# Optimization experiments

Measured on AMD Instinct MI355X. Metric: run time of the kernel, lower is better.

Reference implementation:

```python
import jax, jax.numpy as jnp
import numpy as np

DECAY = 0.95

def setup_inputs() -> dict:
    key = jax.random.key(0)
    k1, k2, k3, k4 = jax.random.split(key, 4)
    B, S, H, Dk, Dv = 4, 4096, 16, 64, 64
    return {
        "memory": jax.random.normal(k1, (H, Dk, Dv), dtype=jnp.float32),
        "keys": jax.random.normal(k2, (B, S, H, Dk), dtype=jnp.float32),
        "values": jax.random.normal(k3, (B, S, H, Dv), dtype=jnp.float32),
        "write_strengths": jax.random.uniform(k4, (B, S), dtype=jnp.float32),
    }

def reference(memory, keys, values, write_strengths):
    # M_new = decay * M + sum_{b,s} rho[b,s] * k[b,s,h] v[b,s,h]^T
    # Algebraically equivalent to per-head (rho-weighted) K^T V contraction;
    # avoids materializing the (B,S,H,Dk,Dv) outer-product tensor.
    delta = jnp.einsum('bs,bshk,bshv->hkv', write_strengths, keys, values)
    return DECAY * memory + delta
```

## Files before the change

### kernel.cpp

```cpp
#include <hip/hip_runtime.h>


typedef __bf16  bf16x8  __attribute__((ext_vector_type(8)));
typedef float   floatx4 __attribute__((ext_vector_type(4)));

constexpr int HH = 16;
constexpr int DK = 64;
constexpr int DV = 64;
constexpr int ROWS = 16384;
constexpr int NSLICE = 64;
constexpr int RPB = ROWS / NSLICE;
constexpr int RPW = RPB / 4;
constexpr int TS  = 32;
constexpr int NT  = RPW / TS;
constexpr int PAD = 65;
constexpr float DECAY = 0.95f;
constexpr size_t WS_NEED = (size_t)NSLICE * HH * DK * DV * 4;

__global__ __launch_bounds__(256) void init_out(const float* __restrict__ mem,
                                                float* __restrict__ out) {
    int i = blockIdx.x * 256 + threadIdx.x;
    out[i] = DECAY * mem[i];
}

__global__ __launch_bounds__(256) void accum(const float* __restrict__ keys,
                                             const float* __restrict__ values,
                                             const float* __restrict__ rho,
                                             float* __restrict__ out,
                                             float* __restrict__ ws,
                                             int use_ws) {
    __shared__ float red[2][64 * PAD];

    const int t    = threadIdx.x;
    const int w    = t >> 6;
    const int lane = t & 63;
    const int m15  = lane & 15;
    const int q    = lane >> 4;
    const int h    = blockIdx.y;
    const int row0 = blockIdx.x * RPB + w * RPW;

    floatx4 acc[4][4];
    #pragma unroll
    for (int i = 0; i < 4; ++i)
        #pragma unroll
        for (int j = 0; j < 4; ++j)
            acc[i][j] = (floatx4){0.f, 0.f, 0.f, 0.f};

    #pragma unroll
    for (int tile = 0; tile < NT; ++tile) {
        const int s0 = row0 + tile * TS;
        const int sl = s0 + q * 8;

        float4 r0 = *(const float4*)(rho + sl);
        float4 r1 = *(const float4*)(rho + sl + 4);
        float rv[8] = {r0.x, r0.y, r0.z, r0.w, r1.x, r1.y, r1.z, r1.w};

        const float* kbase = keys   + ((size_t)sl * HH + h) * DK + m15;
        const float* vbase = values + ((size_t)sl * HH + h) * DV + m15;

        bf16x8 af[4], bfr[4];
        #pragma unroll
        for (int mt = 0; mt < 4; ++mt) {
            #pragma unroll
            for (int j = 0; j < 8; ++j) {
                float x = kbase[(size_t)j * (HH * DK) + mt * 16] * rv[j];
                af[mt][j] = (__bf16)x;
            }
        }
        #pragma unroll
        for (int nt = 0; nt < 4; ++nt) {
            #pragma unroll
            for (int j = 0; j < 8; ++j) {
                float x = vbase[(size_t)j * (HH * DV) + nt * 16];
                bfr[nt][j] = (__bf16)x;
            }
        }

        #pragma unroll
        for (int mt = 0; mt < 4; ++mt)
            #pragma unroll
            for (int nt = 0; nt < 4; ++nt)
                acc[mt][nt] = __builtin_amdgcn_mfma_f32_16x16x32_bf16(
                    af[mt], bfr[nt], acc[mt][nt], 0, 0, 0);
    }

    float* dst = red[w & 1];
    if (w < 2) {
        #pragma unroll
        for (int mt = 0; mt < 4; ++mt)
            #pragma unroll
            for (int nt = 0; nt < 4; ++nt)
                #pragma unroll
                for (int r = 0; r < 4; ++r)
                    dst[(mt * 16 + q * 4 + r) * PAD + nt * 16 + m15] = acc[mt][nt][r];
    }
    __syncthreads();
    if (w >= 2) {
        #pragma unroll
        for (int mt = 0; mt < 4; ++mt)
            #pragma unroll
            for (int nt = 0; nt < 4; ++nt)
                #pragma unroll
                for (int r = 0; r < 4; ++r) {
                    float* p = &dst[(mt * 16 + q * 4 + r) * PAD + nt * 16 + m15];
                    *p = *p + acc[mt][nt][r];
                }
    }
    __syncthreads();

    if (use_ws) {
        float* wsp = ws + ((size_t)blockIdx.x * HH + h) * (DK * DV);
        #pragma unroll
        for (int i = 0; i < 16; ++i) {
            int idx = i * 256 + t;
            int rr = idx >> 6, cc = idx & 63;
            wsp[idx] = red[0][rr * PAD + cc] + red[1][rr * PAD + cc];
        }
    } else {
        float* o = out + h * (DK * DV);
        #pragma unroll
        for (int i = 0; i < 16; ++i) {
            int idx = i * 256 + t;
            int rr = idx >> 6, cc = idx & 63;
            atomicAdd(o + idx, red[0][rr * PAD + cc] + red[1][rr * PAD + cc]);
        }
    }
}

__global__ __launch_bounds__(256) void reduce_ws(const float* __restrict__ mem,
                                                 const float* __restrict__ ws,
                                                 float* __restrict__ out) {
    const int o4 = blockIdx.x * 256 + threadIdx.x;
    const int o  = o4 * 4;
    const int h  = o >> 12;
    const int i  = o & 4095;

    float4 m = *(const float4*)(mem + o);
    float4 acc = make_float4(DECAY * m.x, DECAY * m.y, DECAY * m.z, DECAY * m.w);

    const float* p = ws + (size_t)h * (DK * DV) + i;
    #pragma unroll 8
    for (int c = 0; c < NSLICE; ++c) {
        float4 v = *(const float4*)(p + (size_t)c * HH * DK * DV);
        acc.x += v.x; acc.y += v.y; acc.z += v.z; acc.w += v.w;
    }
    *(float4*)(out + o) = acc;
}

extern "C" void kernel_launch(void* const* d_in, const int* in_sizes, int n_in,
                              void* d_out, int out_size, void* d_ws, size_t ws_size,
                              hipStream_t stream) {
    const float* mem    = (const float*)d_in[0];
    const float* keys   = (const float*)d_in[1];
    const float* values = (const float*)d_in[2];
    const float* rho    = (const float*)d_in[3];
    float* out = (float*)d_out;
    float* ws  = (float*)d_ws;

    dim3 grid(NSLICE, HH);
    if (ws_size >= WS_NEED) {
        accum<<<grid, dim3(256), 0, stream>>>(keys, values, rho, out, ws, 1);
        reduce_ws<<<dim3(64), dim3(256), 0, stream>>>(mem, ws, out);
    } else {
        init_out<<<dim3((HH * DK * DV) / 256), dim3(256), 0, stream>>>(mem, out);
        accum<<<grid, dim3(256), 0, stream>>>(keys, values, rho, out, ws, 0);
    }
}
```

Before: 166.8 us.

## Stage K/V tiles through LDS using vectorized float4 global loads

The old scalar strided global loads of keys and values become per-lane float4 loads. Each wave scales keys by rho, packs the data to bf16, and writes it to a private padded LDS tile, then reads the MFMA fragments back from LDS. The second tile's global loads are issued before the first tile's MFMAs so memory latency overlaps compute. The LDS buffer is reused for the cross-wave reduction after a barrier. This cuts the number of load instructions and memory transactions, at the cost of extra LDS traffic and register pressure from holding two tiles of prefetched data.

```diff
diff --git a/kernel.cpp b/kernel.cpp
--- a/kernel.cpp
+++ b/kernel.cpp
@@ -11,8 +11,9 @@
 constexpr int NSLICE = 64;
 constexpr int RPB = ROWS / NSLICE;
 constexpr int RPW = RPB / 4;
-constexpr int TS  = 32;
-constexpr int NT  = RPW / TS;
+constexpr int TSR = 32;
+constexpr int SPW = 68;
+constexpr int WAVE_DW = 2 * TSR * SPW / 2;
 constexpr int PAD = 65;
 constexpr float DECAY = 0.95f;
 constexpr size_t WS_NEED = (size_t)NSLICE * HH * DK * DV * 4;
@@ -21,6 +22,13 @@
                                                 float* __restrict__ out) {
     int i = blockIdx.x * 256 + threadIdx.x;
     out[i] = DECAY * mem[i];
+}
+
+__device__ __forceinline__ unsigned int pk2(float a, float b) {
+    __bf16 lo = (__bf16)a, hi = (__bf16)b;
+    unsigned short ul = __builtin_bit_cast(unsigned short, lo);
+    unsigned short uh = __builtin_bit_cast(unsigned short, hi);
+    return (unsigned int)ul | ((unsigned int)uh << 16);
 }
 
 __global__ __launch_bounds__(256) void accum(const float* __restrict__ keys,
@@ -29,7 +37,7 @@
                                              float* __restrict__ out,
                                              float* __restrict__ ws,
                                              int use_ws) {
-    __shared__ float red[2][64 * PAD];
+    __shared__ __align__(16) unsigned char smem_raw[34816];
 
     const int t    = threadIdx.x;
     const int w    = t >> 6;
@@ -39,6 +47,9 @@
     const int h    = blockIdx.y;
     const int row0 = blockIdx.x * RPB + w * RPW;
 
+    unsigned short* kb = (unsigned short*)smem_raw + (size_t)w * WAVE_DW * 2;
+    unsigned short* vb = kb + TSR * SPW;
+
     floatx4 acc[4][4];
     #pragma unroll
     for (int i = 0; i < 4; ++i)
@@ -46,45 +57,73 @@
         for (int j = 0; j < 4; ++j)
             acc[i][j] = (floatx4){0.f, 0.f, 0.f, 0.f};
 
-    #pragma unroll
-    for (int tile = 0; tile < NT; ++tile) {
-        const int s0 = row0 + tile * TS;
-        const int sl = s0 + q * 8;
-
-        float4 r0 = *(const float4*)(rho + sl);
-        float4 r1 = *(const float4*)(rho + sl + 4);
-        float rv[8] = {r0.x, r0.y, r0.z, r0.w, r1.x, r1.y, r1.z, r1.w};
-
-        const float* kbase = keys   + ((size_t)sl * HH + h) * DK + m15;
-        const float* vbase = values + ((size_t)sl * HH + h) * DV + m15;
-
-        bf16x8 af[4], bfr[4];
-        #pragma unroll
-        for (int mt = 0; mt < 4; ++mt) {
-            #pragma unroll
-            for (int j = 0; j < 8; ++j) {
-                float x = kbase[(size_t)j * (HH * DK) + mt * 16] * rv[j];
-                af[mt][j] = (__bf16)x;
-            }
-        }
-        #pragma unroll
-        for (int nt = 0; nt < 4; ++nt) {
-            #pragma unroll
-            for (int j = 0; j < 8; ++j) {
-                float x = vbase[(size_t)j * (HH * DV) + nt * 16];
-                bfr[nt][j] = (__bf16)x;
-            }
-        }
-
-        #pragma unroll
-        for (int mt = 0; mt < 4; ++mt)
-            #pragma unroll
-            for (int nt = 0; nt < 4; ++nt)
-                acc[mt][nt] = __builtin_amdgcn_mfma_f32_16x16x32_bf16(
-                    af[mt], bfr[nt], acc[mt][nt], 0, 0, 0);
-    }
-
-    float* dst = red[w & 1];
+    const size_t rstride = (size_t)HH * DK;
+    const float* kbase = keys   + ((size_t)row0 * HH + h) * DK + m15 * 4;
+    const float* vbase = values + ((size_t)row0 * HH + h) * DV + m15 * 4;
+
+    #define LOADT(T, GK, GV, R0, R1) do {                                     \
+        const float* kp_ = kbase + (size_t)((T) * TSR + q * 8) * rstride;     \
+        const float* vp_ = vbase + (size_t)((T) * TSR + q * 8) * rstride;     \
+        _Pragma("unroll")                                                     \
+        for (int i_ = 0; i_ < 8; ++i_)                                        \
+            GK[i_] = *(const float4*)(kp_ + (size_t)i_ * rstride);            \
+        _Pragma("unroll")                                                     \
+        for (int i_ = 0; i_ < 8; ++i_)                                        \
+            GV[i_] = *(const float4*)(vp_ + (size_t)i_ * rstride);            \
+        R0 = *(const float4*)(rho + row0 + (T) * TSR + q * 8);                \
+        R1 = *(const float4*)(rho + row0 + (T) * TSR + q * 8 + 4);            \
+    } while (0)
+
+    #define STAGE(GK, GV, R0, R1) do {                                        \
+        float rr_[8] = {R0.x, R0.y, R0.z, R0.w, R1.x, R1.y, R1.z, R1.w};      \
+        _Pragma("unroll")                                                     \
+        for (int i_ = 0; i_ < 8; ++i_) {                                      \
+            float4 x_ = GK[i_]; float rv_ = rr_[i_];                          \
+            uint2 pk_; pk_.x = pk2(x_.x * rv_, x_.y * rv_);                   \
+            pk_.y = pk2(x_.z * rv_, x_.w * rv_);                              \
+            *(uint2*)(kb + (q * 8 + i_) * SPW + m15 * 4) = pk_;               \
+            float4 y_ = GV[i_];                                               \
+            uint2 pv_; pv_.x = pk2(y_.x, y_.y); pv_.y = pk2(y_.z, y_.w);      \
+            *(uint2*)(vb + (q * 8 + i_) * SPW + m15 * 4) = pv_;               \
+        }                                                                     \
+    } while (0)
+
+    #define FRAGMM() do {                                                     \
+        bf16x8 af_[4], bv_[4];                                                \
+        _Pragma("unroll")                                                     \
+        for (int mt_ = 0; mt_ < 4; ++mt_)                                     \
+            _Pragma("unroll")                                                 \
+            for (int j_ = 0; j_ < 8; ++j_) {                                  \
+                af_[mt_][j_] = ((const __bf16*)kb)[(q * 8 + j_) * SPW + m15 + 16 * mt_]; \
+                bv_[mt_][j_] = ((const __bf16*)vb)[(q * 8 + j_) * SPW + m15 + 16 * mt_]; \
+            }                                                                 \
+        _Pragma("unroll")                                                     \
+        for (int mt_ = 0; mt_ < 4; ++mt_)                                     \
+            _Pragma("unroll")                                                 \
+            for (int nt_ = 0; nt_ < 4; ++nt_)                                 \
+                acc[mt_][nt_] = __builtin_amdgcn_mfma_f32_16x16x32_bf16(      \
+                    af_[mt_], bv_[nt_], acc[mt_][nt_], 0, 0, 0);              \
+    } while (0)
+
+    {
+        float4 gk[8], gv[8], r0, r1;
+        float4 hk[8], hv[8], s0, s1;
+        LOADT(0, gk, gv, r0, r1);
+        STAGE(gk, gv, r0, r1);
+        LOADT(1, hk, hv, s0, s1);
+        FRAGMM();
+        STAGE(hk, hv, s0, s1);
+        FRAGMM();
+    }
+    #undef LOADT
+    #undef STAGE
+    #undef FRAGMM
+
+    __syncthreads();
+    float* red0 = (float*)smem_raw;
+    float* red1 = red0 + 64 * PAD;
+    float* dst  = (w & 1) ? red1 : red0;
+
     if (w < 2) {
         #pragma unroll
         for (int mt = 0; mt < 4; ++mt)
@@ -114,7 +153,7 @@
         for (int i = 0; i < 16; ++i) {
             int idx = i * 256 + t;
             int rr = idx >> 6, cc = idx & 63;
-            wsp[idx] = red[0][rr * PAD + cc] + red[1][rr * PAD + cc];
+            wsp[idx] = red0[rr * PAD + cc] + red1[rr * PAD + cc];
         }
     } else {
         float* o = out + h * (DK * DV);
@@ -122,7 +161,7 @@
         for (int i = 0; i < 16; ++i) {
             int idx = i * 256 + t;
             int rr = idx >> 6, cc = idx & 63;
-            atomicAdd(o + idx, red[0][rr * PAD + cc] + red[1][rr * PAD + cc]);
+            atomicAdd(o + idx, red0[rr * PAD + cc] + red1[rr * PAD + cc]);
         }
     }
 }
```

After: 163.5 us. 1.02x faster.
